# Performance work log

Hardware: AMD Instinct MI355X
Metric: run time of the kernel (lower is better)

The kernel has to match this reference:

```python
import jax, jax.numpy as jnp
import numpy as np

N_NODES = 50000
N_EDGES = 800000
IN_FEATS, HIDDEN_FEATS, NUM_CLASSES = 64, 64, 32


def setup_inputs() -> dict:
    key = jax.random.key(0)
    ks = jax.random.split(key, 9)
    features = jax.random.normal(ks[0], (N_NODES, IN_FEATS), dtype=jnp.float32)
    src = jax.random.randint(ks[1], (N_EDGES,), 0, N_NODES, dtype=jnp.int32)
    dst = jax.random.randint(ks[2], (N_EDGES,), 0, N_NODES, dtype=jnp.int32)
    def lin(k, fan_in, fan_out):
        bound = 1.0 / np.sqrt(fan_in)
        return jax.random.uniform(k, (fan_in, fan_out), jnp.float32, -bound, bound)
    W_self1 = lin(ks[3], IN_FEATS, HIDDEN_FEATS)
    W_neigh1 = lin(ks[4], IN_FEATS, HIDDEN_FEATS)
    b1 = jnp.zeros((HIDDEN_FEATS,), jnp.float32)
    W_self2 = lin(ks[5], HIDDEN_FEATS, NUM_CLASSES)
    W_neigh2 = lin(ks[6], HIDDEN_FEATS, NUM_CLASSES)
    b2 = jnp.zeros((NUM_CLASSES,), jnp.float32)
    return {"features": features, "W_self1": W_self1, "W_neigh1": W_neigh1, "b1": b1,
            "W_self2": W_self2, "W_neigh2": W_neigh2, "b2": b2, "src": src, "dst": dst}


def _sage_mean(x, W_self, W_neigh, b, src, dst, n_nodes):
    # mean over in-neighbors: edge (u, v) sends x[u] into v
    agg = jax.ops.segment_sum(x[src], dst, num_segments=n_nodes)          # [N, F]
    deg = jax.ops.segment_sum(jnp.ones((src.shape[0],), x.dtype), dst,
                              num_segments=n_nodes)                        # [N]
    h_neigh = agg / jnp.maximum(deg, 1.0)[:, None]                         # zero-in-degree -> 0
    return x @ W_self + h_neigh @ W_neigh + b


def reference(features, W_self1, W_neigh1, b1, W_self2, W_neigh2, b2, src, dst):
    n = features.shape[0]
    h = jax.nn.relu(_sage_mean(features, W_self1, W_neigh1, b1, src, dst, n))
    return _sage_mean(h, W_self2, W_neigh2, b2, src, dst, n)
```

## Files before the change

### kernel.cpp

```cpp
#include <hip/hip_runtime.h>

#define N_NODES 50000
#define N_EDGES 800000
#define NB 196
#define PBLOCKS 256
#define CHUNK 3125
#define GEMM_BLOCKS 782

typedef unsigned short ushort_t;
typedef __attribute__((ext_vector_type(8))) short bf16x8;
typedef __attribute__((ext_vector_type(4))) float f32x4;

__device__ __forceinline__ float bflo(unsigned int u) {
    return __uint_as_float(u << 16);
}
__device__ __forceinline__ float bfhi(unsigned int u) {
    return __uint_as_float(u & 0xffff0000u);
}
__device__ __forceinline__ ushort_t f2bf(float f) {
    unsigned int x = __float_as_uint(f);
    return (ushort_t)((x + 0x7fffu + ((x >> 16) & 1u)) >> 16);
}
__device__ __forceinline__ unsigned int pack_bf(float lo, float hi) {
    return (unsigned int)f2bf(lo) | ((unsigned int)f2bf(hi) << 16);
}
__device__ __forceinline__ void split_bf(float v, short& hi, short& lo) {
    ushort_t h = f2bf(v);
    float r = v - __uint_as_float((unsigned int)h << 16);
    hi = (short)h;
    lo = (short)f2bf(r);
}

__global__ __launch_bounds__(256)
void gemm128_and_count(const float* __restrict__ A,
                       const float* __restrict__ B1,
                       const float* __restrict__ B2,
                       ushort_t* __restrict__ Cself,
                       ushort_t* __restrict__ Cn,
                       const int* __restrict__ dst,
                       int* __restrict__ blocktot) {
    __shared__ int hist[NB];

    if (blockIdx.x >= GEMM_BLOCKS) {
        const int pb = blockIdx.x - GEMM_BLOCKS;
        for (int i = threadIdx.x; i < NB; i += 256) hist[i] = 0;
        __syncthreads();
        const int e0 = pb * CHUNK;
        const int e1 = e0 + CHUNK;
        for (int e = e0 + (int)threadIdx.x; e < e1; e += 256)
            atomicAdd(&hist[dst[e] >> 8], 1);
        __syncthreads();
        for (int i = threadIdx.x; i < NB; i += 256)
            blocktot[i * PBLOCKS + pb] = hist[i];
        return;
    }

    const int l  = threadIdx.x & 63;
    const int w  = threadIdx.x >> 6;
    const int lr = l & 15;
    const int lk = (l >> 4) << 3;

    bf16x8 bhi[2][2], blo[2][2];
#pragma unroll
    for (int nt = 0; nt < 2; ++nt) {
        const int n = w * 32 + nt * 16 + lr;
        const float* Bp = (n < 64) ? (B1 + n) : (B2 + (n - 64));
#pragma unroll
        for (int ks = 0; ks < 2; ++ks) {
#pragma unroll
            for (int j = 0; j < 8; ++j) {
                float bv = Bp[(size_t)(ks * 32 + lk + j) * 64];
                short h, lo;
                split_bf(bv, h, lo);
                bhi[nt][ks][j] = h;
                blo[nt][ks][j] = lo;
            }
        }
    }

    const int m0 = blockIdx.x * 64;
    f32x4 acc[4][2];
#pragma unroll
    for (int mt = 0; mt < 4; ++mt)
#pragma unroll
        for (int nt = 0; nt < 2; ++nt) {
            f32x4 z = {0.f, 0.f, 0.f, 0.f};
            acc[mt][nt] = z;
        }

#pragma unroll
    for (int mt = 0; mt < 4; ++mt) {
        const int m = m0 + mt * 16 + lr;
        const bool valid = (m < N_NODES);
        const float* Ap = A + (size_t)m * 64 + lk;
#pragma unroll
        for (int ks = 0; ks < 2; ++ks) {
            float4 f0, f1;
            if (valid) {
                f0 = *(const float4*)(Ap + ks * 32);
                f1 = *(const float4*)(Ap + ks * 32 + 4);
            } else {
                f0 = make_float4(0.f, 0.f, 0.f, 0.f);
                f1 = f0;
            }
            const float fv[8] = {f0.x, f0.y, f0.z, f0.w, f1.x, f1.y, f1.z, f1.w};
            bf16x8 ahi, alo;
#pragma unroll
            for (int j = 0; j < 8; ++j) {
                short h, lo;
                split_bf(fv[j], h, lo);
                ahi[j] = h;
                alo[j] = lo;
            }
#pragma unroll
            for (int nt = 0; nt < 2; ++nt) {
                acc[mt][nt] = __builtin_amdgcn_mfma_f32_16x16x32_bf16(
                    ahi, bhi[nt][ks], acc[mt][nt], 0, 0, 0);
                acc[mt][nt] = __builtin_amdgcn_mfma_f32_16x16x32_bf16(
                    alo, bhi[nt][ks], acc[mt][nt], 0, 0, 0);
                acc[mt][nt] = __builtin_amdgcn_mfma_f32_16x16x32_bf16(
                    ahi, blo[nt][ks], acc[mt][nt], 0, 0, 0);
            }
        }
    }

#pragma unroll
    for (int mt = 0; mt < 4; ++mt) {
        const int mbase = m0 + mt * 16 + ((l >> 4) << 2);
#pragma unroll
        for (int nt = 0; nt < 2; ++nt) {
            const int n = w * 32 + nt * 16 + lr;
            ushort_t* T = (n < 64) ? (Cself + n) : (Cn + (n - 64));
#pragma unroll
            for (int r = 0; r < 4; ++r) {
                const int m = mbase + r;
                if (m < N_NODES) T[(size_t)m * 64] = f2bf(acc[mt][nt][r]);
            }
        }
    }
}

__global__ __launch_bounds__(256)
void part_write(const int* __restrict__ src, const int* __restrict__ dst,
                const int* __restrict__ blocktot, unsigned int* __restrict__ brec) {
    __shared__ int ssum[256];
    __shared__ int cur[NB];
    const int pb = blockIdx.x;
    const int t  = threadIdx.x;

    int rsum = 0, mypart = 0;
    if (t < NB) {
        const int* rp = blocktot + t * PBLOCKS;
#pragma unroll 8
        for (int j = 0; j < PBLOCKS; ++j) {
            if (j == pb) mypart = rsum;
            rsum += rp[j];
        }
    }
    ssum[t] = (t < NB) ? rsum : 0;
    __syncthreads();
    for (int off = 1; off < 256; off <<= 1) {
        int add = (t >= off) ? ssum[t - off] : 0;
        __syncthreads();
        ssum[t] += add;
        __syncthreads();
    }
    if (t < NB) cur[t] = (ssum[t] - rsum) + mypart;
    __syncthreads();

    const int e0 = pb * CHUNK;
    const int e1 = e0 + CHUNK;
    for (int e = e0 + t; e < e1; e += 256) {
        int d = dst[e];
        int s = src[e];
        int pos = atomicAdd(&cur[d >> 8], 1);
        brec[pos] = ((unsigned int)(d & 255) << 16) | (unsigned int)s;
    }
}

__global__ __launch_bounds__(256)
void bucket_fill(const int* __restrict__ blocktot,
                 const unsigned int* __restrict__ brec,
                 int* __restrict__ csr_src, int* __restrict__ row_ptr) {
    __shared__ int ssum[256];
    __shared__ int cnt[256];
    __shared__ int cur[256];
    const int b = blockIdx.x;
    const int node0 = b * 256;
    const int t = threadIdx.x;

    int rsum = 0;
    if (t < NB) {
        const int* rp = blocktot + t * PBLOCKS;
#pragma unroll 8
        for (int j = 0; j < PBLOCKS; ++j) rsum += rp[j];
    }
    ssum[t] = (t < NB) ? rsum : 0;
    __syncthreads();
    for (int off = 1; off < 256; off <<= 1) {
        int add = (t >= off) ? ssum[t - off] : 0;
        __syncthreads();
        ssum[t] += add;
        __syncthreads();
    }
    const int w0 = (b == 0) ? 0 : ssum[b - 1];
    const int w1 = ssum[b];
    __syncthreads();

    cnt[t] = 0;
    __syncthreads();
    for (int i = w0 + t; i < w1; i += 256)
        atomicAdd(&cnt[brec[i] >> 16], 1);
    __syncthreads();
    const int v = cnt[t];
    cur[t] = v;
    __syncthreads();
    for (int off = 1; off < 256; off <<= 1) {
        int add = (t >= off) ? cur[t - off] : 0;
        __syncthreads();
        cur[t] += add;
        __syncthreads();
    }
    const int excl = cur[t] - v;
    const int node = node0 + t;
    if (node <= N_NODES) row_ptr[node] = w0 + excl;
    __syncthreads();
    cur[t] = w0 + excl;
    __syncthreads();
    for (int i = w0 + t; i < w1; i += 256) {
        unsigned int r = brec[i];
        int pos = atomicAdd(&cur[r >> 16], 1);
        csr_src[pos] = (int)(r & 0xffffu);
    }
}

__global__ __launch_bounds__(256)
void gemm_cat64_bf16(const ushort_t* __restrict__ A,
                     const float* __restrict__ B1,
                     const float* __restrict__ B2,
                     ushort_t* __restrict__ Cself,
                     ushort_t* __restrict__ Cn) {
    const int l  = threadIdx.x & 63;
    const int w  = threadIdx.x >> 6;
    const int lr = l & 15;
    const int lk = (l >> 4) << 3;

    const int n = w * 16 + lr;
    const float* Bp = (n < 32) ? (B1 + n) : (B2 + (n - 32));
    bf16x8 bhi[2], blo[2];
#pragma unroll
    for (int ks = 0; ks < 2; ++ks) {
#pragma unroll
        for (int j = 0; j < 8; ++j) {
            float bv = Bp[(size_t)(ks * 32 + lk + j) * 32];
            short h, lo;
            split_bf(bv, h, lo);
            bhi[ks][j] = h;
            blo[ks][j] = lo;
        }
    }

    const int m0 = blockIdx.x * 64;
    f32x4 acc[4];
#pragma unroll
    for (int mt = 0; mt < 4; ++mt) {
        f32x4 z = {0.f, 0.f, 0.f, 0.f};
        acc[mt] = z;
    }

#pragma unroll
    for (int mt = 0; mt < 4; ++mt) {
        const int m = m0 + mt * 16 + lr;
        const bool valid = (m < N_NODES);
#pragma unroll
        for (int ks = 0; ks < 2; ++ks) {
            bf16x8 a;
            if (valid) {
                a = *(const bf16x8*)&A[(size_t)m * 64 + ks * 32 + lk];
            } else {
                bf16x8 z = {0, 0, 0, 0, 0, 0, 0, 0};
                a = z;
            }
            acc[mt] = __builtin_amdgcn_mfma_f32_16x16x32_bf16(a, bhi[ks], acc[mt], 0, 0, 0);
            acc[mt] = __builtin_amdgcn_mfma_f32_16x16x32_bf16(a, blo[ks], acc[mt], 0, 0, 0);
        }
    }

    ushort_t* T = (n < 32) ? (Cself + n) : (Cn + (n - 32));
#pragma unroll
    for (int mt = 0; mt < 4; ++mt) {
        const int mbase = m0 + mt * 16 + ((l >> 4) << 2);
#pragma unroll
        for (int r = 0; r < 4; ++r) {
            const int m = mbase + r;
            if (m < N_NODES) T[(size_t)m * 32] = f2bf(acc[mt][r]);
        }
    }
}

template <int F, bool RELU, bool OBF16>
__global__ __launch_bounds__(256)
void gather_epilogue(const ushort_t* __restrict__ Tself,
                     const ushort_t* __restrict__ Tn,
                     const int* __restrict__ row_ptr,
                     const int* __restrict__ csr_src, const float* __restrict__ bias,
                     void* __restrict__ outv) {
    constexpr int LPR  = F / 8;
    constexpr int G    = 32 / LPR;
    constexpr int MAXJ = 32 / G;
    const int lane = threadIdx.x & 63;
    const int half = lane >> 5;
    const int hl   = lane & 31;
    const int r = hl / LPR;
    const int c = hl % LPR;
    const int v = (((int)blockIdx.x * (int)blockDim.x + (int)threadIdx.x) >> 6) * 2 + half;
    if (v >= N_NODES) return;
    const int start = row_ptr[v];
    const int cnt   = row_ptr[v + 1] - start;

    float a[8];
#pragma unroll
    for (int i = 0; i < 8; ++i) a[i] = 0.f;

#define ACC8(u)                                           \
    a[0] += bflo(u.x); a[1] += bfhi(u.x);                 \
    a[2] += bflo(u.y); a[3] += bfhi(u.y);                 \
    a[4] += bflo(u.z); a[5] += bfhi(u.z);                 \
    a[6] += bflo(u.w); a[7] += bfhi(u.w);

    int idx = 0;
    if (hl < cnt) idx = csr_src[start + hl];

    const int nfast = (cnt < 32) ? cnt : 32;
    int  sidx[MAXJ];
    bool act[MAXJ];
#pragma unroll
    for (int j = 0; j < MAXJ; ++j) {
        const int t = r + j * G;
        act[j]  = (t < nfast);
        sidx[j] = __shfl(idx, half * 32 + t);
    }
    uint4 u[MAXJ];
#pragma unroll
    for (int j = 0; j < MAXJ; ++j) {
        u[j] = make_uint4(0u, 0u, 0u, 0u);
        if (act[j]) u[j] = *(const uint4*)&Tn[(size_t)sidx[j] * F + c * 8];
    }
#pragma unroll
    for (int j = 0; j < MAXJ; ++j) { ACC8(u[j]) }

    for (int t = 32 + r; t < cnt; t += G) {
        const int s = csr_src[start + t];
        uint4 uu = *(const uint4*)&Tn[(size_t)s * F + c * 8];
        ACC8(uu)
    }
#undef ACC8

#pragma unroll
    for (int off = LPR; off < 32; off <<= 1) {
#pragma unroll
        for (int i = 0; i < 8; ++i) a[i] += __shfl_xor(a[i], off);
    }

    if (r == 0) {
        const float inv = 1.0f / (float)max(cnt, 1);
        uint4 su = *(const uint4*)&Tself[(size_t)v * F + c * 8];
        float4 bA = *(const float4*)&bias[c * 8];
        float4 bB = *(const float4*)&bias[c * 8 + 4];
        float o[8];
        o[0] = bflo(su.x) + a[0] * inv + bA.x;
        o[1] = bfhi(su.x) + a[1] * inv + bA.y;
        o[2] = bflo(su.y) + a[2] * inv + bA.z;
        o[3] = bfhi(su.y) + a[3] * inv + bA.w;
        o[4] = bflo(su.z) + a[4] * inv + bB.x;
        o[5] = bfhi(su.z) + a[5] * inv + bB.y;
        o[6] = bflo(su.w) + a[6] * inv + bB.z;
        o[7] = bfhi(su.w) + a[7] * inv + bB.w;
        if (RELU) {
#pragma unroll
            for (int i = 0; i < 8; ++i) o[i] = fmaxf(o[i], 0.f);
        }
        if (OBF16) {
            ushort_t* out = (ushort_t*)outv;
            uint4 p;
            p.x = pack_bf(o[0], o[1]); p.y = pack_bf(o[2], o[3]);
            p.z = pack_bf(o[4], o[5]); p.w = pack_bf(o[6], o[7]);
            *(uint4*)&out[(size_t)v * F + c * 8] = p;
        } else {
            float* out = (float*)outv;
            *(float4*)&out[(size_t)v * F + c * 8]     = make_float4(o[0], o[1], o[2], o[3]);
            *(float4*)&out[(size_t)v * F + c * 8 + 4] = make_float4(o[4], o[5], o[6], o[7]);
        }
    }
}

extern "C" void kernel_launch(void* const* d_in, const int* in_sizes, int n_in,
                              void* d_out, int out_size, void* d_ws, size_t ws_size,
                              hipStream_t stream) {
    const float* features = (const float*)d_in[0];
    const float* W_self1  = (const float*)d_in[1];
    const float* W_neigh1 = (const float*)d_in[2];
    const float* b1       = (const float*)d_in[3];
    const float* W_self2  = (const float*)d_in[4];
    const float* W_neigh2 = (const float*)d_in[5];
    const float* b2       = (const float*)d_in[6];
    const int*   src      = (const int*)d_in[7];
    const int*   dst      = (const int*)d_in[8];

    ushort_t* Tself1 = (ushort_t*)d_ws;
    ushort_t* Tn1    = Tself1 + (size_t)N_NODES * 64;
    ushort_t* h      = Tn1 + (size_t)N_NODES * 64;
    int* row_ptr     = (int*)(h + (size_t)N_NODES * 64);
    int* csr_src     = row_ptr + (N_NODES + 1);
    unsigned int* brec = (unsigned int*)(csr_src + N_EDGES);
    int* blocktot    = (int*)(brec + N_EDGES);

    ushort_t* Tself2 = Tself1;
    ushort_t* Tn2    = Tself1 + (size_t)N_NODES * 32;

    const int gather_blocks = (N_NODES + 7) / 8;

    gemm128_and_count<<<GEMM_BLOCKS + PBLOCKS, 256, 0, stream>>>(
        features, W_self1, W_neigh1, Tself1, Tn1, dst, blocktot);
    part_write<<<PBLOCKS, 256, 0, stream>>>(src, dst, blocktot, brec);
    bucket_fill<<<NB, 256, 0, stream>>>(blocktot, brec, csr_src, row_ptr);
    gather_epilogue<64, true, true><<<gather_blocks, 256, 0, stream>>>(
        Tself1, Tn1, row_ptr, csr_src, b1, h);
    gemm_cat64_bf16<<<GEMM_BLOCKS, 256, 0, stream>>>(h, W_self2, W_neigh2, Tself2, Tn2);
    gather_epilogue<32, false, false><<<gather_blocks, 256, 0, stream>>>(
        Tself2, Tn2, row_ptr, csr_src, b2, d_out);
}
```

Baseline: 164.3 us.

## Replace CSR build and per-node gather with bucketed LDS-atomic aggregation

Drops the bucket_fill kernel that built a full CSR, and the per-node gather over row_ptr/csr_src. Each of the 196 buckets now runs one 1024-thread block that streams its bucket's edge records, gathers neighbour rows and accumulates them into a shared-memory float tile with LDS atomics, counting degree in shared memory too, then applies the mean/self/bias epilogue. This removes one launch and the CSR scatter pass. In exchange it adds heavy LDS atomic traffic and runs only 196 large blocks, which may underfill the GPU and makes the float summation order nondeterministic.

```diff
diff --git a/kernel.cpp b/kernel.cpp
--- a/kernel.cpp
+++ b/kernel.cpp
@@ -29,6 +29,9 @@
     float r = v - __uint_as_float((unsigned int)h << 16);
     hi = (short)h;
     lo = (short)f2bf(r);
+}
+__device__ __forceinline__ void lds_faddf(float* p, float v) {
+    __hip_atomic_fetch_add(p, v, __ATOMIC_RELAXED, __HIP_MEMORY_SCOPE_WORKGROUP);
 }
 
 __global__ __launch_bounds__(256)
@@ -142,7 +145,8 @@
 
 __global__ __launch_bounds__(256)
 void part_write(const int* __restrict__ src, const int* __restrict__ dst,
-                const int* __restrict__ blocktot, unsigned int* __restrict__ brec) {
+                const int* __restrict__ blocktot, unsigned int* __restrict__ brec,
+                int* __restrict__ bucketstart) {
     __shared__ int ssum[256];
     __shared__ int cur[NB];
     const int pb = blockIdx.x;
@@ -165,7 +169,12 @@
         ssum[t] += add;
         __syncthreads();
     }
-    if (t < NB) cur[t] = (ssum[t] - rsum) + mypart;
+    if (t < NB) {
+        const int w0 = ssum[t] - rsum;
+        cur[t] = w0 + mypart;
+        if (pb == 0) bucketstart[t] = w0;
+    }
+    if (pb == 0 && t == 0) bucketstart[NB] = N_EDGES;
     __syncthreads();
 
     const int e0 = pb * CHUNK;
@@ -178,59 +187,98 @@
     }
 }
 
-__global__ __launch_bounds__(256)
-void bucket_fill(const int* __restrict__ blocktot,
-                 const unsigned int* __restrict__ brec,
-                 int* __restrict__ csr_src, int* __restrict__ row_ptr) {
-    __shared__ int ssum[256];
-    __shared__ int cnt[256];
-    __shared__ int cur[256];
+template <int F, bool RELU, bool OBF16>
+__global__ __launch_bounds__(1024)
+void gather_lds(const ushort_t* __restrict__ Tself,
+                const ushort_t* __restrict__ Tn,
+                const unsigned int* __restrict__ brec,
+                const int* __restrict__ bucketstart,
+                const float* __restrict__ bias,
+                void* __restrict__ outv) {
+    constexpr int LPR = F / 8;
+    constexpr int NG  = 1024 / LPR;
+    constexpr int ST  = F + 2;
+    __shared__ float acc[256 * ST];
+    __shared__ int hist[256];
+
     const int b = blockIdx.x;
-    const int node0 = b * 256;
     const int t = threadIdx.x;
-
-    int rsum = 0;
-    if (t < NB) {
-        const int* rp = blocktot + t * PBLOCKS;
-#pragma unroll 8
-        for (int j = 0; j < PBLOCKS; ++j) rsum += rp[j];
-    }
-    ssum[t] = (t < NB) ? rsum : 0;
+    const int w0 = bucketstart[b];
+    const int w1 = bucketstart[b + 1];
+
+    for (int i = t; i < 256 * ST; i += 1024) acc[i] = 0.f;
+    if (t < 256) hist[t] = 0;
     __syncthreads();
-    for (int off = 1; off < 256; off <<= 1) {
-        int add = (t >= off) ? ssum[t - off] : 0;
-        __syncthreads();
-        ssum[t] += add;
-        __syncthreads();
-    }
-    const int w0 = (b == 0) ? 0 : ssum[b - 1];
-    const int w1 = ssum[b];
+
+    const int g  = t / LPR;
+    const int c  = t % LPR;
+    const int cb = c * 8;
+
+#define ADD8(d, u) { float* p = &acc[(d) * ST + cb];                \
+    lds_faddf(p + 0, bflo(u.x)); lds_faddf(p + 1, bfhi(u.x));       \
+    lds_faddf(p + 2, bflo(u.y)); lds_faddf(p + 3, bfhi(u.y));       \
+    lds_faddf(p + 4, bflo(u.z)); lds_faddf(p + 5, bfhi(u.z));       \
+    lds_faddf(p + 6, bflo(u.w)); lds_faddf(p + 7, bfhi(u.w)); }
+
+    int i = w0 + g;
+    for (; i + 3 * NG < w1; i += 4 * NG) {
+        const unsigned int r0 = brec[i];
+        const unsigned int r1 = brec[i + NG];
+        const unsigned int r2 = brec[i + 2 * NG];
+        const unsigned int r3 = brec[i + 3 * NG];
+        const uint4 u0 = *(const uint4*)&Tn[(size_t)(r0 & 0xffffu) * F + cb];
+        const uint4 u1 = *(const uint4*)&Tn[(size_t)(r1 & 0xffffu) * F + cb];
+        const uint4 u2 = *(const uint4*)&Tn[(size_t)(r2 & 0xffffu) * F + cb];
+        const uint4 u3 = *(const uint4*)&Tn[(size_t)(r3 & 0xffffu) * F + cb];
+        if (c == 0) {
+            atomicAdd(&hist[r0 >> 16], 1); atomicAdd(&hist[r1 >> 16], 1);
+            atomicAdd(&hist[r2 >> 16], 1); atomicAdd(&hist[r3 >> 16], 1);
+        }
+        ADD8(r0 >> 16, u0) ADD8(r1 >> 16, u1) ADD8(r2 >> 16, u2) ADD8(r3 >> 16, u3)
+    }
+    for (; i < w1; i += NG) {
+        const unsigned int r = brec[i];
+        const uint4 u = *(const uint4*)&Tn[(size_t)(r & 0xffffu) * F + cb];
+        if (c == 0) atomicAdd(&hist[r >> 16], 1);
+        ADD8(r >> 16, u)
+    }
+#undef ADD8
     __syncthreads();
 
-    cnt[t] = 0;
-    __syncthreads();
-    for (int i = w0 + t; i < w1; i += 256)
-        atomicAdd(&cnt[brec[i] >> 16], 1);
-    __syncthreads();
-    const int v = cnt[t];
-    cur[t] = v;
-    __syncthreads();
-    for (int off = 1; off < 256; off <<= 1) {
-        int add = (t >= off) ? cur[t - off] : 0;
-        __syncthreads();
-        cur[t] += add;
-        __syncthreads();
-    }
-    const int excl = cur[t] - v;
-    const int node = node0 + t;
-    if (node <= N_NODES) row_ptr[node] = w0 + excl;
-    __syncthreads();
-    cur[t] = w0 + excl;
-    __syncthreads();
-    for (int i = w0 + t; i < w1; i += 256) {
-        unsigned int r = brec[i];
-        int pos = atomicAdd(&cur[r >> 16], 1);
-        csr_src[pos] = (int)(r & 0xffffu);
+#pragma unroll
+    for (int nn = 0; nn < 256 / NG; ++nn) {
+        const int d = g + nn * NG;
+        const int v = b * 256 + d;
+        if (v >= N_NODES) continue;
+        const float inv = 1.0f / (float)max(hist[d], 1);
+        const uint4 su = *(const uint4*)&Tself[(size_t)v * F + cb];
+        const float4 bA = *(const float4*)&bias[cb];
+        const float4 bB = *(const float4*)&bias[cb + 4];
+        const float* p = &acc[d * ST + cb];
+        float o[8];
+        o[0] = bflo(su.x) + p[0] * inv + bA.x;
+        o[1] = bfhi(su.x) + p[1] * inv + bA.y;
+        o[2] = bflo(su.y) + p[2] * inv + bA.z;
+        o[3] = bfhi(su.y) + p[3] * inv + bA.w;
+        o[4] = bflo(su.z) + p[4] * inv + bB.x;
+        o[5] = bfhi(su.z) + p[5] * inv + bB.y;
+        o[6] = bflo(su.w) + p[6] * inv + bB.z;
+        o[7] = bfhi(su.w) + p[7] * inv + bB.w;
+        if (RELU) {
+#pragma unroll
+            for (int k = 0; k < 8; ++k) o[k] = fmaxf(o[k], 0.f);
+        }
+        if (OBF16) {
+            ushort_t* out = (ushort_t*)outv;
+            uint4 pk;
+            pk.x = pack_bf(o[0], o[1]); pk.y = pack_bf(o[2], o[3]);
+            pk.z = pack_bf(o[4], o[5]); pk.w = pack_bf(o[6], o[7]);
+            *(uint4*)&out[(size_t)v * F + cb] = pk;
+        } else {
+            float* out = (float*)outv;
+            *(float4*)&out[(size_t)v * F + cb]     = make_float4(o[0], o[1], o[2], o[3]);
+            *(float4*)&out[(size_t)v * F + cb + 4] = make_float4(o[4], o[5], o[6], o[7]);
+        }
     }
 }
 
@@ -294,102 +342,6 @@
         for (int r = 0; r < 4; ++r) {
             const int m = mbase + r;
             if (m < N_NODES) T[(size_t)m * 32] = f2bf(acc[mt][r]);
-        }
-    }
-}
-
-template <int F, bool RELU, bool OBF16>
-__global__ __launch_bounds__(256)
-void gather_epilogue(const ushort_t* __restrict__ Tself,
-                     const ushort_t* __restrict__ Tn,
-                     const int* __restrict__ row_ptr,
-                     const int* __restrict__ csr_src, const float* __restrict__ bias,
-                     void* __restrict__ outv) {
-    constexpr int LPR  = F / 8;
-    constexpr int G    = 32 / LPR;
-    constexpr int MAXJ = 32 / G;
-    const int lane = threadIdx.x & 63;
-    const int half = lane >> 5;
-    const int hl   = lane & 31;
-    const int r = hl / LPR;
-    const int c = hl % LPR;
-    const int v = (((int)blockIdx.x * (int)blockDim.x + (int)threadIdx.x) >> 6) * 2 + half;
-    if (v >= N_NODES) return;
-    const int start = row_ptr[v];
-    const int cnt   = row_ptr[v + 1] - start;
-
-    float a[8];
-#pragma unroll
-    for (int i = 0; i < 8; ++i) a[i] = 0.f;
-
-#define ACC8(u)                                           \
-    a[0] += bflo(u.x); a[1] += bfhi(u.x);                 \
-    a[2] += bflo(u.y); a[3] += bfhi(u.y);                 \
-    a[4] += bflo(u.z); a[5] += bfhi(u.z);                 \
-    a[6] += bflo(u.w); a[7] += bfhi(u.w);
-
-    int idx = 0;
-    if (hl < cnt) idx = csr_src[start + hl];
-
-    const int nfast = (cnt < 32) ? cnt : 32;
-    int  sidx[MAXJ];
-    bool act[MAXJ];
-#pragma unroll
-    for (int j = 0; j < MAXJ; ++j) {
-        const int t = r + j * G;
-        act[j]  = (t < nfast);
-        sidx[j] = __shfl(idx, half * 32 + t);
-    }
-    uint4 u[MAXJ];
-#pragma unroll
-    for (int j = 0; j < MAXJ; ++j) {
-        u[j] = make_uint4(0u, 0u, 0u, 0u);
-        if (act[j]) u[j] = *(const uint4*)&Tn[(size_t)sidx[j] * F + c * 8];
-    }
-#pragma unroll
-    for (int j = 0; j < MAXJ; ++j) { ACC8(u[j]) }
-
-    for (int t = 32 + r; t < cnt; t += G) {
-        const int s = csr_src[start + t];
-        uint4 uu = *(const uint4*)&Tn[(size_t)s * F + c * 8];
-        ACC8(uu)
-    }
-#undef ACC8
-
-#pragma unroll
-    for (int off = LPR; off < 32; off <<= 1) {
-#pragma unroll
-        for (int i = 0; i < 8; ++i) a[i] += __shfl_xor(a[i], off);
-    }
-
-    if (r == 0) {
-        const float inv = 1.0f / (float)max(cnt, 1);
-        uint4 su = *(const uint4*)&Tself[(size_t)v * F + c * 8];
-        float4 bA = *(const float4*)&bias[c * 8];
-        float4 bB = *(const float4*)&bias[c * 8 + 4];
-        float o[8];
-        o[0] = bflo(su.x) + a[0] * inv + bA.x;
-        o[1] = bfhi(su.x) + a[1] * inv + bA.y;
-        o[2] = bflo(su.y) + a[2] * inv + bA.z;
-        o[3] = bfhi(su.y) + a[3] * inv + bA.w;
-        o[4] = bflo(su.z) + a[4] * inv + bB.x;
-        o[5] = bfhi(su.z) + a[5] * inv + bB.y;
-        o[6] = bflo(su.w) + a[6] * inv + bB.z;
-        o[7] = bfhi(su.w) + a[7] * inv + bB.w;
-        if (RELU) {
-#pragma unroll
-            for (int i = 0; i < 8; ++i) o[i] = fmaxf(o[i], 0.f);
-        }
-        if (OBF16) {
-            ushort_t* out = (ushort_t*)outv;
-            uint4 p;
-            p.x = pack_bf(o[0], o[1]); p.y = pack_bf(o[2], o[3]);
-            p.z = pack_bf(o[4], o[5]); p.w = pack_bf(o[6], o[7]);
-            *(uint4*)&out[(size_t)v * F + c * 8] = p;
-        } else {
-            float* out = (float*)outv;
-            *(float4*)&out[(size_t)v * F + c * 8]     = make_float4(o[0], o[1], o[2], o[3]);
-            *(float4*)&out[(size_t)v * F + c * 8 + 4] = make_float4(o[4], o[5], o[6], o[7]);
         }
     }
 }
@@ -410,23 +362,19 @@
     ushort_t* Tself1 = (ushort_t*)d_ws;
     ushort_t* Tn1    = Tself1 + (size_t)N_NODES * 64;
     ushort_t* h      = Tn1 + (size_t)N_NODES * 64;
-    int* row_ptr     = (int*)(h + (size_t)N_NODES * 64);
-    int* csr_src     = row_ptr + (N_NODES + 1);
-    unsigned int* brec = (unsigned int*)(csr_src + N_EDGES);
+    unsigned int* brec = (unsigned int*)(h + (size_t)N_NODES * 64);
     int* blocktot    = (int*)(brec + N_EDGES);
+    int* bucketstart = blocktot + NB * PBLOCKS;
 
     ushort_t* Tself2 = Tself1;
     ushort_t* Tn2    = Tself1 + (size_t)N_NODES * 32;
 
-    const int gather_blocks = (N_NODES + 7) / 8;
-
     gemm128_and_count<<<GEMM_BLOCKS + PBLOCKS, 256, 0, stream>>>(
         features, W_self1, W_neigh1, Tself1, Tn1, dst, blocktot);
-    part_write<<<PBLOCKS, 256, 0, stream>>>(src, dst, blocktot, brec);
-    bucket_fill<<<NB, 256, 0, stream>>>(blocktot, brec, csr_src, row_ptr);
-    gather_epilogue<64, true, true><<<gather_blocks, 256, 0, stream>>>(
-        Tself1, Tn1, row_ptr, csr_src, b1, h);
+    part_write<<<PBLOCKS, 256, 0, stream>>>(src, dst, blocktot, brec, bucketstart);
+    gather_lds<64, true, true><<<NB, 1024, 0, stream>>>(
+        Tself1, Tn1, brec, bucketstart, b1, h);
     gemm_cat64_bf16<<<GEMM_BLOCKS, 256, 0, stream>>>(h, W_self2, W_neigh2, Tself2, Tn2);
-    gather_epilogue<32, false, false><<<gather_blocks, 256, 0, stream>>>(
-        Tself2, Tn2, row_ptr, csr_src, b2, d_out);
-}
+    gather_lds<32, false, false><<<NB, 1024, 0, stream>>>(
+        Tself2, Tn2, brec, bucketstart, b2, d_out);
+}
```

Result: slower. 637.1 us (+287.6%).
